# Kernel tuning notes

Measured on AMD Instinct MI355X. Metric: run time of the kernel, lower is better.

The kernel has to match this reference:

```python
import jax, jax.numpy as jnp
import numpy as np

B, H, I, S = 4096, 2048, 2048, 3
TAU = 1.0
LN_EPS = 1e-5
SC = 0.02  # weight init scale to keep tanh/sigmoid in a sane range


def setup_inputs() -> dict:
    key = jax.random.key(0)
    ks = jax.random.split(key, 10)
    # precomputed Gumbel(0,1) noise for gumbel_softmax (deterministic reference)
    u = jax.random.uniform(ks[3], (B, S), minval=1e-6, maxval=1.0 - 1e-6)
    gumbel = -jnp.log(-jnp.log(u))
    return {
        "x": jax.random.normal(ks[0], (B, I), dtype=jnp.float32),
        "prev_master_h": jax.random.normal(ks[1], (B, H), dtype=jnp.float32),
        "prev_sub_h": jax.random.normal(ks[2], (S, B, H), dtype=jnp.float32),
        "gumbel": gumbel.astype(jnp.float32),
        "W_ih": jax.random.normal(ks[4], (S, H, I), dtype=jnp.float32) * SC,
        "W_hh": jax.random.normal(ks[5], (S, H, H), dtype=jnp.float32) * SC,
        "b_ih": jnp.zeros((S, H), dtype=jnp.float32),
        "b_hh": jnp.zeros((S, H), dtype=jnp.float32),
        "gate_W": jax.random.normal(ks[6], (S, H), dtype=jnp.float32) * SC,
        "gate_b": jnp.zeros((S,), dtype=jnp.float32),
        "fusion_W": jax.random.normal(ks[7], (H, H), dtype=jnp.float32) * SC,
        "fusion_b": jnp.zeros((H,), dtype=jnp.float32),
        "ln_g": jnp.ones((H,), dtype=jnp.float32),
        "ln_b": jnp.zeros((H,), dtype=jnp.float32),
    }


def reference(x, prev_master_h, prev_sub_h, gumbel, W_ih, W_hh, b_ih, b_hh,
              gate_W, gate_b, fusion_W, fusion_b, ln_g, ln_b):
    # gate logits: Linear(hidden -> num_sub), torch Linear is x @ W.T + b
    logits = prev_master_h @ gate_W.T + gate_b              # [B, S]
    # hard gumbel-softmax with straight-through estimator
    y_soft = jax.nn.softmax((logits + gumbel) / TAU, axis=-1)
    y_hard = jax.nn.one_hot(jnp.argmax(y_soft, axis=-1), S, dtype=y_soft.dtype)
    gate = y_hard + y_soft - jax.lax.stop_gradient(y_soft)  # [B, S]
    # vectorized vanilla RNN sub-cells: tanh(x W_ih^T + h W_hh^T + b)
    new_sub = jnp.tanh(
        jnp.einsum('bi,shi->sbh', x, W_ih)
        + jnp.einsum('sbi,shi->sbh', prev_sub_h, W_hh)
        + b_ih[:, None, :] + b_hh[:, None, :]
    )                                                        # [S, B, H]
    # hard one-hot mixture of sub-cell states
    weighted = jnp.einsum('bs,sbh->bh', gate, new_sub)       # [B, H]
    fused = weighted @ fusion_W.T + fusion_b                 # [B, H]
    pre = prev_master_h + fused
    mu = jnp.mean(pre, axis=-1, keepdims=True)
    var = jnp.mean(jnp.square(pre - mu), axis=-1, keepdims=True)
    normed = (pre - mu) * jax.lax.rsqrt(var + LN_EPS) * ln_g + ln_b
    master_h_new = jax.nn.sigmoid(normed)
    return master_h_new, gate, new_sub
```

## Files before the change

kernel.cpp:

```cpp
#include <hip/hip_runtime.h>
#include <cstdint>
#include <cstddef>

#define B_SZ 4096
#define H_SZ 2048
#define S_SZ 3

typedef __attribute__((ext_vector_type(8))) _Float16 f16x8;
typedef __attribute__((ext_vector_type(4))) float f32x4;

__device__ __forceinline__ void glds16(const void* g, void* l) {
    __builtin_amdgcn_global_load_lds(
        (const __attribute__((address_space(1))) void*)g,
        (__attribute__((address_space(3))) void*)l, 16, 0, 0);
}

__device__ __forceinline__ float wave_red_sum(float v) {
#pragma unroll
    for (int off = 32; off > 0; off >>= 1) v += __shfl_down(v, off);
    return v;
}

__global__ __launch_bounds__(256) void cvt_f16_kernel(
    const float* __restrict__ src, _Float16* __restrict__ dst, int n4)
{
    const int i = blockIdx.x * 256 + threadIdx.x;
    if (i >= n4) return;
    const float4 v = ((const float4*)src)[i];
    _Float16 h[4];
    h[0] = (_Float16)v.x; h[1] = (_Float16)v.y;
    h[2] = (_Float16)v.z; h[3] = (_Float16)v.w;
    *(uint2*)(dst + (size_t)i * 4) = *(const uint2*)h;
}

__global__ __launch_bounds__(64) void gate_kernel(
    const float* __restrict__ prev_master, const float* __restrict__ gate_W,
    const float* __restrict__ gate_b, const float* __restrict__ gumbel,
    float* __restrict__ out_gate)
{
    const int b = blockIdx.x;
    const int lane = threadIdx.x;
    const float* row = prev_master + (size_t)b * H_SZ;
    double a0 = 0.0, a1 = 0.0, a2 = 0.0;
#pragma unroll
    for (int k = lane * 4; k < H_SZ; k += 64 * 4) {
        float4 v  = *(const float4*)(row + k);
        float4 w0 = *(const float4*)(gate_W + 0 * H_SZ + k);
        float4 w1 = *(const float4*)(gate_W + 1 * H_SZ + k);
        float4 w2 = *(const float4*)(gate_W + 2 * H_SZ + k);
        a0 += (double)v.x * w0.x + (double)v.y * w0.y + (double)v.z * w0.z + (double)v.w * w0.w;
        a1 += (double)v.x * w1.x + (double)v.y * w1.y + (double)v.z * w1.z + (double)v.w * w1.w;
        a2 += (double)v.x * w2.x + (double)v.y * w2.y + (double)v.z * w2.z + (double)v.w * w2.w;
    }
#pragma unroll
    for (int off = 32; off > 0; off >>= 1) {
        a0 += __shfl_down(a0, off);
        a1 += __shfl_down(a1, off);
        a2 += __shfl_down(a2, off);
    }
    if (lane == 0) {
        float z0 = (float)a0 + gate_b[0] + gumbel[b * 3 + 0];
        float z1 = (float)a1 + gate_b[1] + gumbel[b * 3 + 1];
        float z2 = (float)a2 + gate_b[2] + gumbel[b * 3 + 2];
        float zm = fmaxf(z0, fmaxf(z1, z2));
        float e0 = expf(z0 - zm), e1 = expf(z1 - zm), e2 = expf(z2 - zm);
        float se = e0 + e1 + e2;
        float y0 = e0 / se, y1 = e1 / se, y2 = e2 / se;
        int am = 0; float best = y0;
        if (y1 > best) { best = y1; am = 1; }
        if (y2 > best) { best = y2; am = 2; }
        float h0 = (am == 0) ? 1.0f : 0.0f;
        float h1 = (am == 1) ? 1.0f : 0.0f;
        float h2 = (am == 2) ? 1.0f : 0.0f;
        out_gate[b * 3 + 0] = (h0 + y0) - y0;
        out_gate[b * 3 + 1] = (h1 + y1) - y1;
        out_gate[b * 3 + 2] = (h2 + y2) - y2;
    }
}

__global__ __launch_bounds__(256) void sub_gemm_kernel(
    const _Float16* __restrict__ x16, const _Float16* __restrict__ sub16,
    const _Float16* __restrict__ Wih16, const _Float16* __restrict__ Whh16,
    const float* __restrict__ b_ih, const float* __restrict__ b_hh,
    float* __restrict__ out_new_sub)
{
    const int s  = blockIdx.z;
    const int n0 = blockIdx.x * 128;
    const int m0 = blockIdx.y * 128;

    __shared__ __align__(16) _Float16 lds_a[128 * 32];
    __shared__ __align__(16) _Float16 lds_w[128 * 32];

    const int tid  = threadIdx.x;
    const int lane = tid & 63;
    const int wave = tid >> 6;
    const int wm = (wave >> 1) * 64;
    const int wn = (wave & 1) * 64;
    const int lrow = lane & 15;
    const int lc   = lane >> 4;
    const int fcol = (lc ^ ((lrow >> 1) & 3)) * 8;

    const int srow   = lane >> 2;
    const int schunk = (lane & 3) ^ ((lane >> 3) & 3);

    f32x4 acc[4][4] = {};

    for (int phase = 0; phase < 2; ++phase) {
        const _Float16* Asrc = phase ? (sub16 + (size_t)s * B_SZ * 2048) : x16;
        const _Float16* Wsrc = (phase ? Whh16 : Wih16) + (size_t)s * H_SZ * 2048;
        for (int kt = 0; kt < 2048; kt += 32) {
#pragma unroll
            for (int t = 0; t < 2; ++t) {
                const int rb = wave * 32 + t * 16;
                glds16(Asrc + (size_t)(m0 + rb + srow) * 2048 + kt + schunk * 8,
                       &lds_a[rb * 32]);
                glds16(Wsrc + (size_t)(n0 + rb + srow) * 2048 + kt + schunk * 8,
                       &lds_w[rb * 32]);
            }
            __syncthreads();
            f16x8 af[4], wf[4];
#pragma unroll
            for (int i = 0; i < 4; ++i) {
                af[i] = *(const f16x8*)&lds_a[(wm + i * 16 + lrow) * 32 + fcol];
                wf[i] = *(const f16x8*)&lds_w[(wn + i * 16 + lrow) * 32 + fcol];
            }
#pragma unroll
            for (int i = 0; i < 4; ++i)
#pragma unroll
                for (int j = 0; j < 4; ++j)
                    acc[i][j] = __builtin_amdgcn_mfma_f32_16x16x32_f16(af[i], wf[j], acc[i][j], 0, 0, 0);
            __syncthreads();
        }
    }
#pragma unroll
    for (int j = 0; j < 4; ++j) {
        const int n = n0 + wn + j * 16 + lrow;
        const float bias = b_ih[s * H_SZ + n] + b_hh[s * H_SZ + n];
#pragma unroll
        for (int i = 0; i < 4; ++i) {
            const int mbase = m0 + wm + i * 16 + (lane >> 4) * 4;
#pragma unroll
            for (int r = 0; r < 4; ++r) {
                const int m = mbase + r;
                out_new_sub[((size_t)s * B_SZ + m) * H_SZ + n] = tanhf(acc[i][j][r] + bias);
            }
        }
    }
}

__global__ __launch_bounds__(256) void weighted_kernel(
    const float* __restrict__ new_sub, const float* __restrict__ gate,
    _Float16* __restrict__ w16)
{
    const size_t p = (size_t)blockIdx.x * 256 + threadIdx.x;
    const size_t b = p / (H_SZ / 4);
    const int h4 = (int)(p % (H_SZ / 4)) * 4;
    const float g0 = gate[b * 3 + 0], g1 = gate[b * 3 + 1], g2 = gate[b * 3 + 2];
    const float4 v0 = *(const float4*)(new_sub + ((size_t)0 * B_SZ + b) * H_SZ + h4);
    const float4 v1 = *(const float4*)(new_sub + ((size_t)1 * B_SZ + b) * H_SZ + h4);
    const float4 v2 = *(const float4*)(new_sub + ((size_t)2 * B_SZ + b) * H_SZ + h4);
    _Float16 h[4];
    h[0] = (_Float16)(g0 * v0.x + g1 * v1.x + g2 * v2.x);
    h[1] = (_Float16)(g0 * v0.y + g1 * v1.y + g2 * v2.y);
    h[2] = (_Float16)(g0 * v0.z + g1 * v1.z + g2 * v2.z);
    h[3] = (_Float16)(g0 * v0.w + g1 * v1.w + g2 * v2.w);
    *(uint2*)(w16 + b * H_SZ + h4) = *(const uint2*)h;
}

__global__ __launch_bounds__(256) void fusion_gemm_kernel(
    const _Float16* __restrict__ a16, const _Float16* __restrict__ w16,
    const float* __restrict__ fusion_b, const float* __restrict__ prev_master,
    float* __restrict__ out_pre)
{
    const int n0 = blockIdx.x * 128;
    const int m0 = blockIdx.y * 128;

    __shared__ __align__(16) _Float16 lds_a[128 * 32];
    __shared__ __align__(16) _Float16 lds_w[128 * 32];

    const int tid  = threadIdx.x;
    const int lane = tid & 63;
    const int wave = tid >> 6;
    const int wm = (wave >> 1) * 64;
    const int wn = (wave & 1) * 64;
    const int lrow = lane & 15;
    const int lc   = lane >> 4;
    const int fcol = (lc ^ ((lrow >> 1) & 3)) * 8;
    const int srow   = lane >> 2;
    const int schunk = (lane & 3) ^ ((lane >> 3) & 3);

    f32x4 acc[4][4] = {};

    for (int kt = 0; kt < H_SZ; kt += 32) {
#pragma unroll
        for (int t = 0; t < 2; ++t) {
            const int rb = wave * 32 + t * 16;
            glds16(a16 + (size_t)(m0 + rb + srow) * H_SZ + kt + schunk * 8,
                   &lds_a[rb * 32]);
            glds16(w16 + (size_t)(n0 + rb + srow) * H_SZ + kt + schunk * 8,
                   &lds_w[rb * 32]);
        }
        __syncthreads();
        f16x8 af[4], wf[4];
#pragma unroll
        for (int i = 0; i < 4; ++i) {
            af[i] = *(const f16x8*)&lds_a[(wm + i * 16 + lrow) * 32 + fcol];
            wf[i] = *(const f16x8*)&lds_w[(wn + i * 16 + lrow) * 32 + fcol];
        }
#pragma unroll
        for (int i = 0; i < 4; ++i)
#pragma unroll
            for (int j = 0; j < 4; ++j)
                acc[i][j] = __builtin_amdgcn_mfma_f32_16x16x32_f16(af[i], wf[j], acc[i][j], 0, 0, 0);
        __syncthreads();
    }
#pragma unroll
    for (int j = 0; j < 4; ++j) {
        const int n = n0 + wn + j * 16 + lrow;
        const float fb = fusion_b[n];
#pragma unroll
        for (int i = 0; i < 4; ++i) {
            const int mbase = m0 + wm + i * 16 + (lane >> 4) * 4;
#pragma unroll
            for (int r = 0; r < 4; ++r) {
                const int m = mbase + r;
                out_pre[(size_t)m * H_SZ + n] = acc[i][j][r] + fb + prev_master[(size_t)m * H_SZ + n];
            }
        }
    }
}

__global__ __launch_bounds__(256) void ln_sigmoid_kernel(
    float* __restrict__ master, const float* __restrict__ ln_g,
    const float* __restrict__ ln_b)
{
    const int b = blockIdx.x;
    const int t = threadIdx.x;
    float* row = master + (size_t)b * H_SZ;
    float v[8];
    float4 p0 = *(const float4*)(row + t * 4);
    float4 p1 = *(const float4*)(row + 1024 + t * 4);
    v[0] = p0.x; v[1] = p0.y; v[2] = p0.z; v[3] = p0.w;
    v[4] = p1.x; v[5] = p1.y; v[6] = p1.z; v[7] = p1.w;
    float lsum = 0.f;
#pragma unroll
    for (int e = 0; e < 8; ++e) lsum += v[e];
    __shared__ float red[8];
    float wsum = wave_red_sum(lsum);
    const int lane = t & 63, wid = t >> 6;
    if (lane == 0) red[wid] = wsum;
    __syncthreads();
    const float mu = (red[0] + red[1] + red[2] + red[3]) * (1.0f / H_SZ);
    float lsq = 0.f;
#pragma unroll
    for (int e = 0; e < 8; ++e) { float d = v[e] - mu; lsq += d * d; }
    float wsq = wave_red_sum(lsq);
    if (lane == 0) red[4 + wid] = wsq;
    __syncthreads();
    const float var = (red[4] + red[5] + red[6] + red[7]) * (1.0f / H_SZ);
    const float rs = rsqrtf(var + 1e-5f);
#pragma unroll
    for (int half = 0; half < 2; ++half)
#pragma unroll
        for (int e = 0; e < 4; ++e) {
            const int col = half * 1024 + t * 4 + e;
            const float nm = (v[half * 4 + e] - mu) * rs * ln_g[col] + ln_b[col];
            row[col] = 1.0f / (1.0f + expf(-nm));
        }
}

extern "C" void kernel_launch(void* const* d_in, const int* in_sizes, int n_in,
                              void* d_out, int out_size, void* d_ws, size_t ws_size,
                              hipStream_t stream)
{
    const float* x           = (const float*)d_in[0];
    const float* prev_master = (const float*)d_in[1];
    const float* prev_sub    = (const float*)d_in[2];
    const float* gumbel      = (const float*)d_in[3];
    const float* W_ih        = (const float*)d_in[4];
    const float* W_hh        = (const float*)d_in[5];
    const float* b_ih        = (const float*)d_in[6];
    const float* b_hh        = (const float*)d_in[7];
    const float* gate_W      = (const float*)d_in[8];
    const float* gate_b      = (const float*)d_in[9];
    const float* fusion_W    = (const float*)d_in[10];
    const float* fusion_b    = (const float*)d_in[11];
    const float* ln_g        = (const float*)d_in[12];
    const float* ln_b        = (const float*)d_in[13];

    float* out = (float*)d_out;
    float* out_master  = out;
    float* out_gate    = out + (size_t)B_SZ * H_SZ;
    float* out_new_sub = out_gate + (size_t)B_SZ * S_SZ;

    _Float16* ws = (_Float16*)d_ws;
    _Float16* x16    = ws;
    _Float16* sub16  = x16   + (size_t)B_SZ * H_SZ;
    _Float16* Wih16  = sub16 + (size_t)S_SZ * B_SZ * H_SZ;
    _Float16* Whh16  = Wih16 + (size_t)S_SZ * H_SZ * H_SZ;
    _Float16* fusW16 = Whh16 + (size_t)S_SZ * H_SZ * H_SZ;
    _Float16* wtd16  = fusW16 + (size_t)H_SZ * H_SZ;

    const int n4_x   = B_SZ * H_SZ / 4;
    const int n4_sub = S_SZ * B_SZ * H_SZ / 4;
    const int n4_w   = S_SZ * H_SZ * H_SZ / 4;
    const int n4_fw  = H_SZ * H_SZ / 4;

    cvt_f16_kernel<<<n4_x / 256, 256, 0, stream>>>(x, x16, n4_x);
    cvt_f16_kernel<<<n4_sub / 256, 256, 0, stream>>>(prev_sub, sub16, n4_sub);
    cvt_f16_kernel<<<n4_w / 256, 256, 0, stream>>>(W_ih, Wih16, n4_w);
    cvt_f16_kernel<<<n4_w / 256, 256, 0, stream>>>(W_hh, Whh16, n4_w);
    cvt_f16_kernel<<<n4_fw / 256, 256, 0, stream>>>(fusion_W, fusW16, n4_fw);

    gate_kernel<<<B_SZ, 64, 0, stream>>>(prev_master, gate_W, gate_b, gumbel, out_gate);

    sub_gemm_kernel<<<dim3(H_SZ / 128, B_SZ / 128, S_SZ), 256, 0, stream>>>(
        x16, sub16, Wih16, Whh16, b_ih, b_hh, out_new_sub);

    weighted_kernel<<<(B_SZ * (H_SZ / 4)) / 256, 256, 0, stream>>>(
        out_new_sub, out_gate, wtd16);

    fusion_gemm_kernel<<<dim3(H_SZ / 128, B_SZ / 128), 256, 0, stream>>>(
        wtd16, fusW16, fusion_b, prev_master, out_master);

    ln_sigmoid_kernel<<<B_SZ, 256, 0, stream>>>(out_master, ln_g, ln_b);
}
```

Before: 755.0 us.

## Replace both GEMMs with a multi-buffered, software-pipelined 128x256 tile kernel

Merges the sub-cell GEMM and the fusion GEMM into one templated kernel. It uses 512-thread blocks with 128x256 output tiles and a 5-stage LDS ring filled by async global-to-LDS loads. Fragment reads are double-buffered in registers and waits use explicit vmcnt counts, so loads overlap MFMA work instead of hitting a full barrier every K step. It also remaps the block index for L2 locality and raises MFMA wave priority. The cost is a much larger LDS footprint and higher register pressure, which can limit occupancy, plus hand-counted wait logic that is fragile.

Result: faster. 702.8 us (-6.9%).

```diff
diff --git a/kernel.cpp b/kernel.cpp
--- a/kernel.cpp
+++ b/kernel.cpp
@@ -78,71 +78,127 @@
     }
 }
 
-__global__ __launch_bounds__(256) void sub_gemm_kernel(
-    const _Float16* __restrict__ x16, const _Float16* __restrict__ sub16,
-    const _Float16* __restrict__ Wih16, const _Float16* __restrict__ Whh16,
-    const float* __restrict__ b_ih, const float* __restrict__ b_hh,
-    float* __restrict__ out_new_sub)
-{
-    const int s  = blockIdx.z;
-    const int n0 = blockIdx.x * 128;
-    const int m0 = blockIdx.y * 128;
-
-    __shared__ __align__(16) _Float16 lds_a[128 * 32];
-    __shared__ __align__(16) _Float16 lds_w[128 * 32];
+template<int MODE, int NT>
+__global__ __launch_bounds__(512, 2) void tile_gemm_kernel(
+    const _Float16* __restrict__ A0, const _Float16* __restrict__ A1,
+    const _Float16* __restrict__ W0, const _Float16* __restrict__ W1,
+    const float* __restrict__ bias0, const float* __restrict__ bias1,
+    const float* __restrict__ prev_master, float* __restrict__ out)
+{
+    __shared__ __align__(16) _Float16 lds[5 * 12288];
+
+    const int flat = blockIdx.x;
+    constexpr int QX = (MODE == 0) ? 96 : 32;
+    const int L  = (flat & 7) * QX + (flat >> 3);
+    const int ly = L & 31;
+    const int lx = (L >> 5) & 7;
+    const int s  = (MODE == 0) ? (L >> 8) : 0;
+    const int am0 = ly * 128;
+    const int n0  = lx * 256;
 
     const int tid  = threadIdx.x;
     const int lane = tid & 63;
     const int wave = tid >> 6;
-    const int wm = (wave >> 1) * 64;
-    const int wn = (wave & 1) * 64;
+    const int wm = wave >> 2;
+    const int wn = wave & 3;
     const int lrow = lane & 15;
-    const int lc   = lane >> 4;
-    const int fcol = (lc ^ ((lrow >> 1) & 3)) * 8;
-
-    const int srow   = lane >> 2;
-    const int schunk = (lane & 3) ^ ((lane >> 3) & 3);
+    const int fcol = ((lane >> 4) ^ ((lrow >> 1) & 3)) * 8;
+    const int srow   = tid >> 2;
+    const int schunk = (tid & 3) ^ ((tid >> 3) & 3);
+    const int ldst   = wave << 9;
+
+    int roa[4], rob[4];
+#pragma unroll
+    for (int i = 0; i < 4; ++i) {
+        roa[i] = (wm * 64 + i * 16 + lrow) * 32 + fcol;
+        rob[i] = 4096 + (wn * 64 + i * 16 + lrow) * 32 + fcol;
+    }
 
     f32x4 acc[4][4] = {};
-
-    for (int phase = 0; phase < 2; ++phase) {
-        const _Float16* Asrc = phase ? (sub16 + (size_t)s * B_SZ * 2048) : x16;
-        const _Float16* Wsrc = (phase ? Whh16 : Wih16) + (size_t)s * H_SZ * 2048;
-        for (int kt = 0; kt < 2048; kt += 32) {
-#pragma unroll
-            for (int t = 0; t < 2; ++t) {
-                const int rb = wave * 32 + t * 16;
-                glds16(Asrc + (size_t)(m0 + rb + srow) * 2048 + kt + schunk * 8,
-                       &lds_a[rb * 32]);
-                glds16(Wsrc + (size_t)(n0 + rb + srow) * 2048 + kt + schunk * 8,
-                       &lds_w[rb * 32]);
-            }
-            __syncthreads();
-            f16x8 af[4], wf[4];
-#pragma unroll
-            for (int i = 0; i < 4; ++i) {
-                af[i] = *(const f16x8*)&lds_a[(wm + i * 16 + lrow) * 32 + fcol];
-                wf[i] = *(const f16x8*)&lds_w[(wn + i * 16 + lrow) * 32 + fcol];
-            }
-#pragma unroll
-            for (int i = 0; i < 4; ++i)
-#pragma unroll
-                for (int j = 0; j < 4; ++j)
-                    acc[i][j] = __builtin_amdgcn_mfma_f32_16x16x32_f16(af[i], wf[j], acc[i][j], 0, 0, 0);
-            __syncthreads();
+    f16x8 fAa[4], fAb[4], fBa[4], fBb[4];
+
+    auto stage = [&](int t, int bufe) {
+        int kb; const _Float16 *As, *Ws;
+        if constexpr (MODE == 0) {
+            kb = (t & 63) * 32;
+            if (t < 64) { As = A0;                             Ws = W0 + (size_t)s * (H_SZ * 2048); }
+            else        { As = A1 + (size_t)s * (B_SZ * 2048); Ws = W1 + (size_t)s * (H_SZ * 2048); }
+        } else {
+            kb = t * 32; As = A0; Ws = W0;
         }
-    }
+        const int ko = kb + schunk * 8;
+        glds16(As + (size_t)(am0 + srow)       * 2048 + ko, &lds[bufe + ldst]);
+        glds16(Ws + (size_t)(n0  + srow)       * 2048 + ko, &lds[bufe + 4096 + ldst]);
+        glds16(Ws + (size_t)(n0  + 128 + srow) * 2048 + ko, &lds[bufe + 8192 + ldst]);
+    };
+
+    auto read_frags = [&](int bufe, f16x8 (&fa)[4], f16x8 (&fb)[4]) {
+#pragma unroll
+        for (int i = 0; i < 4; ++i) {
+            fa[i] = *(const f16x8*)&lds[bufe + roa[i]];
+            fb[i] = *(const f16x8*)&lds[bufe + rob[i]];
+        }
+    };
+
+    auto mfma16 = [&](const f16x8 (&fa)[4], const f16x8 (&fb)[4]) {
+        __builtin_amdgcn_s_setprio(1);
+#pragma unroll
+        for (int i = 0; i < 4; ++i)
+#pragma unroll
+            for (int j = 0; j < 4; ++j)
+                acc[i][j] = __builtin_amdgcn_mfma_f32_16x16x32_f16(fa[i], fb[j], acc[i][j], 0, 0, 0);
+        __builtin_amdgcn_s_setprio(0);
+    };
+
+    auto sync_tile = [&](int u) {
+        __builtin_amdgcn_sched_barrier(0);
+        if (u <= NT - 5)      asm volatile("s_waitcnt vmcnt(6)" ::: "memory");
+        else if (u == NT - 4) asm volatile("s_waitcnt vmcnt(3)" ::: "memory");
+        else if (u == NT - 3) asm volatile("s_waitcnt vmcnt(0)" ::: "memory");
+        else return;
+        __builtin_amdgcn_s_barrier();
+        asm volatile("" ::: "memory");
+    };
+
+    stage(0, 0); stage(1, 12288); stage(2, 24576); stage(3, 36864);
+    asm volatile("s_waitcnt vmcnt(6)" ::: "memory");
+    __builtin_amdgcn_s_barrier();
+    asm volatile("" ::: "memory");
+    read_frags(0, fAa, fAb);
+
+    int c = 0;
+    for (int t = 0; t < NT; t += 2) {
+        int b1 = c + 1; if (b1 >= 5) b1 -= 5;
+        int b2 = c + 2; if (b2 >= 5) b2 -= 5;
+        int b4 = c + 4; if (b4 >= 5) b4 -= 5;
+        if (t + 4 < NT) stage(t + 4, b4 * 12288);
+        read_frags(b1 * 12288, fBa, fBb);
+        mfma16(fAa, fAb);
+        sync_tile(t);
+        if (t + 5 < NT) stage(t + 5, c * 12288);
+        if (t + 2 < NT) read_frags(b2 * 12288, fAa, fAb);
+        mfma16(fBa, fBb);
+        sync_tile(t + 1);
+        c += 2; if (c >= 5) c -= 5;
+    }
+
 #pragma unroll
     for (int j = 0; j < 4; ++j) {
-        const int n = n0 + wn + j * 16 + lrow;
-        const float bias = b_ih[s * H_SZ + n] + b_hh[s * H_SZ + n];
+        const int n = n0 + wn * 64 + j * 16 + lrow;
+        float badd;
+        if constexpr (MODE == 0) badd = bias0[s * H_SZ + n] + bias1[s * H_SZ + n];
+        else                     badd = bias0[n];
 #pragma unroll
         for (int i = 0; i < 4; ++i) {
-            const int mbase = m0 + wm + i * 16 + (lane >> 4) * 4;
+            const int mb = am0 + wm * 64 + i * 16 + (lane >> 4) * 4;
 #pragma unroll
             for (int r = 0; r < 4; ++r) {
-                const int m = mbase + r;
-                out_new_sub[((size_t)s * B_SZ + m) * H_SZ + n] = tanhf(acc[i][j][r] + bias);
+                const int m = mb + r;
+                if constexpr (MODE == 0)
+                    out[((size_t)s * B_SZ + m) * H_SZ + n] = tanhf(acc[i][j][r] + badd);
+                else
+                    out[(size_t)m * H_SZ + n] =
+                        acc[i][j][r] + badd + prev_master[(size_t)m * H_SZ + n];
             }
         }
     }
@@ -165,69 +221,6 @@
     h[2] = (_Float16)(g0 * v0.z + g1 * v1.z + g2 * v2.z);
     h[3] = (_Float16)(g0 * v0.w + g1 * v1.w + g2 * v2.w);
     *(uint2*)(w16 + b * H_SZ + h4) = *(const uint2*)h;
-}
-
-__global__ __launch_bounds__(256) void fusion_gemm_kernel(
-    const _Float16* __restrict__ a16, const _Float16* __restrict__ w16,
-    const float* __restrict__ fusion_b, const float* __restrict__ prev_master,
-    float* __restrict__ out_pre)
-{
-    const int n0 = blockIdx.x * 128;
-    const int m0 = blockIdx.y * 128;
-
-    __shared__ __align__(16) _Float16 lds_a[128 * 32];
-    __shared__ __align__(16) _Float16 lds_w[128 * 32];
-
-    const int tid  = threadIdx.x;
-    const int lane = tid & 63;
-    const int wave = tid >> 6;
-    const int wm = (wave >> 1) * 64;
-    const int wn = (wave & 1) * 64;
-    const int lrow = lane & 15;
-    const int lc   = lane >> 4;
-    const int fcol = (lc ^ ((lrow >> 1) & 3)) * 8;
-    const int srow   = lane >> 2;
-    const int schunk = (lane & 3) ^ ((lane >> 3) & 3);
-
-    f32x4 acc[4][4] = {};
-
-    for (int kt = 0; kt < H_SZ; kt += 32) {
-#pragma unroll
-        for (int t = 0; t < 2; ++t) {
-            const int rb = wave * 32 + t * 16;
-            glds16(a16 + (size_t)(m0 + rb + srow) * H_SZ + kt + schunk * 8,
-                   &lds_a[rb * 32]);
-            glds16(w16 + (size_t)(n0 + rb + srow) * H_SZ + kt + schunk * 8,
-                   &lds_w[rb * 32]);
-        }
-        __syncthreads();
-        f16x8 af[4], wf[4];
-#pragma unroll
-        for (int i = 0; i < 4; ++i) {
-            af[i] = *(const f16x8*)&lds_a[(wm + i * 16 + lrow) * 32 + fcol];
-            wf[i] = *(const f16x8*)&lds_w[(wn + i * 16 + lrow) * 32 + fcol];
-        }
-#pragma unroll
-        for (int i = 0; i < 4; ++i)
-#pragma unroll
-            for (int j = 0; j < 4; ++j)
-                acc[i][j] = __builtin_amdgcn_mfma_f32_16x16x32_f16(af[i], wf[j], acc[i][j], 0, 0, 0);
-        __syncthreads();
-    }
-#pragma unroll
-    for (int j = 0; j < 4; ++j) {
-        const int n = n0 + wn + j * 16 + lrow;
-        const float fb = fusion_b[n];
-#pragma unroll
-        for (int i = 0; i < 4; ++i) {
-            const int mbase = m0 + wm + i * 16 + (lane >> 4) * 4;
-#pragma unroll
-            for (int r = 0; r < 4; ++r) {
-                const int m = mbase + r;
-                out_pre[(size_t)m * H_SZ + n] = acc[i][j][r] + fb + prev_master[(size_t)m * H_SZ + n];
-            }
-        }
-    }
 }
 
 __global__ __launch_bounds__(256) void ln_sigmoid_kernel(
@@ -314,14 +307,14 @@
 
     gate_kernel<<<B_SZ, 64, 0, stream>>>(prev_master, gate_W, gate_b, gumbel, out_gate);
 
-    sub_gemm_kernel<<<dim3(H_SZ / 128, B_SZ / 128, S_SZ), 256, 0, stream>>>(
-        x16, sub16, Wih16, Whh16, b_ih, b_hh, out_new_sub);
+    tile_gemm_kernel<0, 128><<<768, 512, 0, stream>>>(
+        x16, sub16, Wih16, Whh16, b_ih, b_hh, nullptr, out_new_sub);
 
     weighted_kernel<<<(B_SZ * (H_SZ / 4)) / 256, 256, 0, stream>>>(
         out_new_sub, out_gate, wtd16);
 
-    fusion_gemm_kernel<<<dim3(H_SZ / 128, B_SZ / 128), 256, 0, stream>>>(
-        wtd16, fusW16, fusion_b, prev_master, out_master);
+    tile_gemm_kernel<1, 64><<<256, 512, 0, stream>>>(
+        wtd16, nullptr, fusW16, nullptr, fusion_b, nullptr, prev_master, out_master);
 
     ln_sigmoid_kernel<<<B_SZ, 256, 0, stream>>>(out_master, ln_g, ln_b);
 }
```
